# Kernel optimization log

Measured on AMD Instinct MI355X. Metric: run time of the kernel, lower is better.

## Reference

```python
import jax, jax.numpy as jnp
import numpy as np

B, S, C, HEADS = 1, 4096, 640, 8
AH, AW = 64, 64            # attn-resolution grid, AH*AW == S
MH, MW = 512, 512          # full-res mask size
NEG = -1e9                 # finite large negative (safe for fully-masked rows)


def nearest_resize(x, h, w):
    # torch F.interpolate(mode='nearest'): idx = floor(i * H_in / H_out)
    H, W = x.shape[-2], x.shape[-1]
    ri = (jnp.arange(h) * H) // h
    ci = (jnp.arange(w) * W) // w
    return x[..., ri, :][..., :, ci]


def sdpa(q, k, v, mask, heads):
    # q,k,v: [B,S,C]; mask: [B,1,S,S] bool (True = attend), broadcasts over heads
    b, s, c = q.shape
    d = c // heads
    qh = q.reshape(b, s, heads, d).transpose(0, 2, 1, 3)  # bhsd
    kh = k.reshape(b, s, heads, d).transpose(0, 2, 1, 3)
    vh = v.reshape(b, s, heads, d).transpose(0, 2, 1, 3)
    scores = jnp.einsum('bhqd,bhkd->bhqk', qh, kh) / jnp.sqrt(jnp.asarray(d, qh.dtype))
    scores = jnp.where(mask, scores, NEG)
    attn = jax.nn.softmax(scores, axis=-1)
    out = jnp.einsum('bhqk,bhkd->bhqd', attn, vh)
    return out.transpose(0, 2, 1, 3).reshape(b, s, c)


def setup_inputs():
    key = jax.random.key(0)
    ks = jax.random.split(key, 14)
    std = 1.0 / np.sqrt(C)
    w = lambda k: (jax.random.normal(k, (C, C), jnp.float32) * std)
    return {
        'hidden_states': jax.random.normal(ks[0], (B, S, C), jnp.float32),
        'mask': jax.random.randint(ks[1], (B, 1, MH, MW), 0, 4, jnp.int32),
        'inpainting_mask': jax.random.randint(ks[2], (B, 1, MH, MW), 0, 2, jnp.int32),
        'Wq': w(ks[3]), 'Wk': w(ks[4]), 'Wv': w(ks[5]),
        'Wq_ent': w(ks[6]), 'Wk_ent': w(ks[7]), 'Wv_ent': w(ks[8]),
        'Wq_out': w(ks[9]), 'Wk_out': w(ks[10]), 'Wv_out': w(ks[11]),
        'Wo': w(ks[12]),
    }


def reference(hidden_states, mask, inpainting_mask, Wq, Wk, Wv,
              Wq_ent, Wk_ent, Wv_ent, Wq_out, Wk_out, Wv_out, Wo):
    residual = hidden_states
    b, s, c = hidden_states.shape

    # --- interpolation-derived masks (kept as [B,1,S,S]; broadcasts over heads) ---
    m = nearest_resize(mask, AH, AW).reshape(b, 1, s)                 # entity labels
    attn_mask = m[:, :, :, None] == m[:, :, None, :]                  # same-entity [B,1,S,S]
    im = nearest_resize(inpainting_mask, AH, AW).reshape(b, 1, s)
    outside_key = (im[:, :, None, :] == 0)                            # [B,1,1,S]
    attn_mask_outside = attn_mask & outside_key                       # [B,1,S,S]

    # --- projections ---
    q = hidden_states @ Wq.T
    k = hidden_states @ Wk.T
    v = hidden_states @ Wv.T
    q_e = hidden_states @ Wq_ent.T
    k_e = hidden_states @ Wk_ent.T
    v_e = hidden_states @ Wv_ent.T
    q_o = hidden_states @ Wq_out.T
    k_o = hidden_states @ Wk_out.T
    v_o = hidden_states @ Wv_out.T

    # --- three SDPA branches ---
    hs_orig = sdpa(q, k, v, attn_mask, HEADS)            # original attention
    hs_ent = sdpa(q_e, k_e, v_e, attn_mask, 1)           # entity attention (1 head)
    hs_out = sdpa(q_o, k_o, v_o, attn_mask_outside, HEADS)  # outside attention

    hs = hs_orig + hs_ent + hs_out
    return hs @ Wo.T + residual
```

## Files before the change

kernel.cpp:

```cpp
#include <hip/hip_runtime.h>
#include <cstdint>

typedef __attribute__((ext_vector_type(8))) short bf16x8;
typedef __attribute__((ext_vector_type(4))) short bf16x4;
typedef __attribute__((ext_vector_type(4))) float f32x4;

#define S_LEN 4096
#define CDIM  640
#define NPROJ 5760

__device__ __forceinline__ f32x4 mfma16(bf16x4 a, bf16x4 b, f32x4 c){
#if defined(__HIP_DEVICE_COMPILE__) && __HIP_DEVICE_COMPILE__
  return __builtin_amdgcn_mfma_f32_16x16x16bf16_1k(a, b, c, 0, 0, 0);
#else
  (void)a; (void)b;
  return c;
#endif
}

__device__ __forceinline__ void gload_lds(const unsigned short* g, unsigned short* l){
#if defined(__HIP_DEVICE_COMPILE__) && __HIP_DEVICE_COMPILE__
  __builtin_amdgcn_global_load_lds((const __attribute__((address_space(1))) unsigned int*)g,
                                   (__attribute__((address_space(3))) unsigned int*)l, 16, 0, 0);
#else
  (void)g; (void)l;
#endif
}

__device__ __forceinline__ unsigned short f2bf(float f){
  union { float f; uint32_t u; } v; v.f = f;
  uint32_t u = v.u;
  return (unsigned short)((u + 0x7fffu + ((u >> 16) & 1u)) >> 16);
}
__device__ __forceinline__ float b2f(unsigned short h){
  union { uint32_t u; float f; } v; v.u = ((uint32_t)h) << 16;
  return v.f;
}

__global__ void k_labels(const int* __restrict__ mask, const int* __restrict__ inp,
                         int* __restrict__ labels){
  int s = blockIdx.x * 256 + threadIdx.x;
  if (s >= S_LEN) return;
  int y = s >> 6, x = s & 63;
  int off = (y * 8) * 512 + x * 8;
  int m = mask[off] & 0xff;
  int o = (inp[off] == 0) ? 0x100 : 0;
  labels[s] = m | o;
}

__global__ void k_hist(const int* __restrict__ labels, int* __restrict__ boff, int* __restrict__ cnt){
  __shared__ int h[4];
  if (threadIdx.x < 4) h[threadIdx.x] = 0;
  __syncthreads();
  for (int s = threadIdx.x; s < S_LEN; s += 256) atomicAdd(&h[labels[s] & 3], 1);
  __syncthreads();
  if (threadIdx.x == 0){
    int a = 0;
    for (int c = 0; c < 4; c++){ boff[c] = a; a += h[c]; }
    boff[4] = a;
  }
  if (threadIdx.x < 4) cnt[threadIdx.x] = 0;
}

__global__ void k_perm(const int* __restrict__ labels, const int* __restrict__ boff,
                       int* __restrict__ cnt, int* __restrict__ perm,
                       int* __restrict__ inv, int* __restrict__ labP){
  int s = blockIdx.x * 256 + threadIdx.x;
  if (s >= S_LEN) return;
  int lab = labels[s];
  int c = lab & 3;
  int pos = boff[c] + atomicAdd(&cnt[c], 1);
  perm[pos] = s; inv[s] = pos; labP[pos] = lab;
}

__global__ void k_tiles(const int* __restrict__ labP, const int* __restrict__ boff,
                        int4* __restrict__ qtinfo, float* __restrict__ rowsum){
  int t = threadIdx.x;
  __shared__ int nkt[32];
  if (t < 32){
    int c0 = labP[t * 128] & 3, c1 = labP[t * 128 + 127] & 3;
    int lo = boff[c0] & ~127, hi = (boff[c1 + 1] + 127) & ~127;
    qtinfo[t].x = lo; qtinfo[t].y = hi; qtinfo[t].w = 0;
    nkt[t] = (hi - lo) >> 7;
  }
  __syncthreads();
  if (t == 0){
    int a = 0;
    for (int i = 0; i < 32; i++){ qtinfo[i].z = a; a += nkt[i]; }
  }
  for (int s = t; s < S_LEN; s += 256) rowsum[s] = 0.f;
}

__global__ void k_cvt_hs(const float* __restrict__ src, unsigned short* __restrict__ dst, int n){
  int idx = (blockIdx.x * 256 + threadIdx.x) * 4;
  if (idx >= n) return;
  float4 v = *(const float4*)(src + idx);
  ushort4 o;
  o.x = f2bf(v.x); o.y = f2bf(v.y); o.z = f2bf(v.z); o.w = f2bf(v.w);
  *(ushort4*)(dst + idx) = o;
}

struct WPtrs { const float* w[10]; };

__global__ void k_cvt_w(WPtrs p, unsigned short* __restrict__ dst){
  int e = (blockIdx.x * 256 + threadIdx.x) * 4;
  if (e >= 10 * 409600) return;
  int a = e / 409600, r = e % 409600;
  float sc = (a == 0 || a == 6) ? 0.11180339887498948f
           : (a == 3 ? 0.03952847075210474f : 1.0f);
  float4 v = *(const float4*)(p.w[a] + r);
  ushort4 o;
  o.x = f2bf(v.x * sc); o.y = f2bf(v.y * sc); o.z = f2bf(v.z * sc); o.w = f2bf(v.w * sc);
  *(ushort4*)(dst + e) = o;
}

template<int EPI>
__global__ __launch_bounds__(256) void k_gemm(const unsigned short* __restrict__ A,
                                              const unsigned short* __restrict__ B,
                                              int M, int N, int K, int ldc,
                                              const int* __restrict__ rowmap,
                                              unsigned short* __restrict__ Cb,
                                              float* __restrict__ Cf,
                                              const float* __restrict__ resid){
  __shared__ __align__(16) unsigned short As[128 * 64];
  __shared__ __align__(16) unsigned short Bs[128 * 64];
  int m0 = blockIdx.y * 128, n0 = blockIdx.x * 128;
  int tid = threadIdx.x;
  int wid = tid >> 6, lane = tid & 63;
  int quad = lane >> 4, l16 = lane & 15;
  int wm = (wid >> 1) * 64, wn = (wid & 1) * 64;
  f32x4 acc[4][4];
#pragma unroll
  for (int i = 0; i < 4; i++)
#pragma unroll
    for (int j = 0; j < 4; j++) acc[i][j] = f32x4{0.f, 0.f, 0.f, 0.f};

  for (int k0 = 0; k0 < K; k0 += 64){
    __syncthreads();
#pragma unroll
    for (int u = 0; u < 4; u++){
      int c = tid + u * 256;
      int row = c >> 3, off = (c & 7) * 8;
      gload_lds(&A[(size_t)(m0 + row) * K + k0 + off], &As[c * 8]);
      gload_lds(&B[(size_t)(n0 + row) * K + k0 + off], &Bs[c * 8]);
    }
    __syncthreads();
#pragma unroll
    for (int ks = 0; ks < 2; ks++){
      bf16x8 af[4], bfr[4];
#pragma unroll
      for (int t = 0; t < 4; t++){
        af[t]  = *(const bf16x8*)(&As[(wm + t * 16 + l16) * 64 + ks * 32 + quad * 8]);
        bfr[t] = *(const bf16x8*)(&Bs[(wn + t * 16 + l16) * 64 + ks * 32 + quad * 8]);
      }
#pragma unroll
      for (int mt = 0; mt < 4; mt++)
#pragma unroll
        for (int nt = 0; nt < 4; nt++)
          acc[mt][nt] = __builtin_amdgcn_mfma_f32_16x16x32_bf16(af[mt], bfr[nt], acc[mt][nt], 0, 0, 0);
    }
  }
#pragma unroll
  for (int mt = 0; mt < 4; mt++)
#pragma unroll
    for (int nt = 0; nt < 4; nt++)
#pragma unroll
      for (int r = 0; r < 4; r++){
        int row = m0 + wm + mt * 16 + quad * 4 + r;
        int col = n0 + wn + nt * 16 + l16;
        float v = acc[mt][nt][r];
        if (EPI == 0){
          Cb[(size_t)rowmap[row] * ldc + col] = f2bf(v);
        } else {
          int ro = rowmap[row];
          Cf[(size_t)ro * ldc + col] = v + resid[(size_t)ro * ldc + col];
        }
      }
}

__global__ void k_transpose_v(const unsigned short* __restrict__ proj, unsigned short* __restrict__ vT){
  __shared__ unsigned short T[64][65];
  int z = blockIdx.z;
  int s0 = blockIdx.x * 64, c0 = blockIdx.y * 64;
  int colbase = 1280 + z * 1920 + c0;
  unsigned short* dst = vT + (size_t)z * CDIM * S_LEN;
  int tid = threadIdx.x;
  for (int i = tid; i < 64 * 64; i += 256){
    int r = i >> 6, c = i & 63;
    T[r][c] = proj[(size_t)(s0 + r) * NPROJ + colbase + c];
  }
  __syncthreads();
  for (int i = tid; i < 64 * 64; i += 256){
    int c = i >> 6, r = i & 63;
    dst[(size_t)(c0 + c) * S_LEN + s0 + r] = T[r][c];
  }
}

#define KP 84
#define VP 76
__global__ __launch_bounds__(256, 2) void k_attn80(const unsigned short* __restrict__ proj,
                                                   const unsigned short* __restrict__ vT,
                                                   const int* __restrict__ labP,
                                                   const int4* __restrict__ qtinfo,
                                                   unsigned short* __restrict__ outP){
  __shared__ __align__(16) unsigned short Ks[2][64 * KP];
  __shared__ __align__(16) unsigned short Vt[2][80 * VP];
  __shared__ __align__(16) int labk[2][64];
  int tid = threadIdx.x, wid = tid >> 6, lane = tid & 63;
  int quad = lane >> 4, l16 = lane & 15;
  int q0 = blockIdx.x * 128;
  int h  = blockIdx.y;
  bool OUTSIDE = (blockIdx.z == 1);
  int qc = (OUTSIDE ? 3840 : 0) + h * 80;
  int kc = (OUTSIDE ? 4480 : 640) + h * 80;
  const unsigned short* vTb = vT + (size_t)(OUTSIDE ? 2 : 0) * CDIM * S_LEN;
  int4 qi = qtinfo[blockIdx.x];
  int t0 = qi.x >> 6, t1 = qi.y >> 6;

  int qrow0 = q0 + wid * 32 + l16;
  int qrow1 = qrow0 + 16;
  bf16x4 qf0[5], qf1[5];
#pragma unroll
  for (int dc = 0; dc < 5; dc++){
    qf0[dc] = *(const bf16x4*)&proj[(size_t)qrow0 * NPROJ + qc + dc * 16 + quad * 4];
    qf1[dc] = *(const bf16x4*)&proj[(size_t)qrow1 * NPROJ + qc + dc * 16 + quad * 4];
  }
  int lq0 = labP[qrow0] & 0xff, lq1 = labP[qrow1] & 0xff;

  float lp0 = 0.f, lp1 = 0.f;
  f32x4 Oc0[5], Oc1[5];
#pragma unroll
  for (int t = 0; t < 5; t++){ Oc0[t] = f32x4{0.f,0.f,0.f,0.f}; Oc1[t] = f32x4{0.f,0.f,0.f,0.f}; }

  const int cS0 = tid, cS1 = tid + 256, cS2 = tid + 512, cS3 = tid + 768, cS4 = tid + 1024;
  const int kga0 = (cS0 / 20) * NPROJ + kc + (cS0 % 20) * 4;
  const int kga1 = (cS1 / 20) * NPROJ + kc + (cS1 % 20) * 4;
  const int kga2 = (cS2 / 20) * NPROJ + kc + (cS2 % 20) * 4;
  const int kga3 = (cS3 / 20) * NPROJ + kc + (cS3 % 20) * 4;
  const int kga4 = (cS4 / 20) * NPROJ + kc + (cS4 % 20) * 4;
  const int kls0 = (cS0 / 20) * KP + (cS0 % 20) * 4;
  const int kls1 = (cS1 / 20) * KP + (cS1 % 20) * 4;
  const int kls2 = (cS2 / 20) * KP + (cS2 % 20) * 4;
  const int kls3 = (cS3 / 20) * KP + (cS3 % 20) * 4;
  const int kls4 = (cS4 / 20) * KP + (cS4 % 20) * 4;
  const int vga0 = (h * 80 + (cS0 >> 4)) * S_LEN + (cS0 & 15) * 4;
  const int vga1 = (h * 80 + (cS1 >> 4)) * S_LEN + (cS1 & 15) * 4;
  const int vga2 = (h * 80 + (cS2 >> 4)) * S_LEN + (cS2 & 15) * 4;
  const int vga3 = (h * 80 + (cS3 >> 4)) * S_LEN + (cS3 & 15) * 4;
  const int vga4 = (h * 80 + (cS4 >> 4)) * S_LEN + (cS4 & 15) * 4;
  const int vls0 = (cS0 >> 4) * VP + (cS0 & 15) * 4;
  const int vls1 = (cS1 >> 4) * VP + (cS1 & 15) * 4;
  const int vls2 = (cS2 >> 4) * VP + (cS2 & 15) * 4;
  const int vls3 = (cS3 >> 4) * VP + (cS3 & 15) * 4;
  const int vls4 = (cS4 >> 4) * VP + (cS4 & 15) * 4;

  uint2 kr0, kr1, kr2, kr3, kr4, vr0, vr1, vr2, vr3, vr4;
  int lreg = 0;

#define LOADT(kt_) do {                                              \
    int _k0 = (kt_) * 64;                                            \
    size_t _kb = (size_t)_k0 * NPROJ;                                \
    kr0 = *(const uint2*)&proj[_kb + kga0];                          \
    kr1 = *(const uint2*)&proj[_kb + kga1];                          \
    kr2 = *(const uint2*)&proj[_kb + kga2];                          \
    kr3 = *(const uint2*)&proj[_kb + kga3];                          \
    kr4 = *(const uint2*)&proj[_kb + kga4];                          \
    vr0 = *(const uint2*)&vTb[(size_t)(vga0 + _k0)];                 \
    vr1 = *(const uint2*)&vTb[(size_t)(vga1 + _k0)];                 \
    vr2 = *(const uint2*)&vTb[(size_t)(vga2 + _k0)];                 \
    vr3 = *(const uint2*)&vTb[(size_t)(vga3 + _k0)];                 \
    vr4 = *(const uint2*)&vTb[(size_t)(vga4 + _k0)];                 \
    if (tid < 64) lreg = labP[_k0 + tid];                            \
  } while (0)

#define WRITET(b) do {                                               \
    *(uint2*)&Ks[b][kls0] = kr0;                                     \
    *(uint2*)&Ks[b][kls1] = kr1;                                     \
    *(uint2*)&Ks[b][kls2] = kr2;                                     \
    *(uint2*)&Ks[b][kls3] = kr3;                                     \
    *(uint2*)&Ks[b][kls4] = kr4;                                     \
    *(uint2*)&Vt[b][vls0] = vr0;                                     \
    *(uint2*)&Vt[b][vls1] = vr1;                                     \
    *(uint2*)&Vt[b][vls2] = vr2;                                     \
    *(uint2*)&Vt[b][vls3] = vr3;                                     \
    *(uint2*)&Vt[b][vls4] = vr4;                                     \
    if (tid < 64) labk[b][tid] = lreg;                               \
  } while (0)

  LOADT(t0);
  WRITET(0);
  if (t0 + 1 < t1) LOADT(t0 + 1);
  __syncthreads();

  int cur = 0;
  for (int kt = t0; kt < t1; kt++){
    int nxt = cur ^ 1;
    if (kt + 1 < t1){
      WRITET(nxt);
      if (kt + 2 < t1) LOADT(kt + 2);
    }

#pragma unroll
    for (int kg = 0; kg < 4; kg++){
      f32x4 sa0 = f32x4{0.f,0.f,0.f,0.f}, sa1 = f32x4{0.f,0.f,0.f,0.f};
#pragma unroll
      for (int dc = 0; dc < 5; dc++){
        bf16x4 kf = *(const bf16x4*)&Ks[cur][(kg * 16 + l16) * KP + dc * 16 + quad * 4];
        sa0 = mfma16(kf, qf0[dc], sa0);
        sa1 = mfma16(kf, qf1[dc], sa1);
      }
      int4 lk4 = *(const int4*)&labk[cur][kg * 16 + quad * 4];
      bool m0 = !OUTSIDE || (lk4.x & 0x100), m1 = !OUTSIDE || (lk4.y & 0x100);
      bool m2 = !OUTSIDE || (lk4.z & 0x100), m3 = !OUTSIDE || (lk4.w & 0x100);
      int k0l = lk4.x & 0xff, k1l = lk4.y & 0xff, k2l = lk4.z & 0xff, k3l = lk4.w & 0xff;
      bf16x4 pf0, pf1;
      {
        float p0 = (k0l == lq0 && m0) ? __expf(sa0[0]) : 0.f;
        float p1 = (k1l == lq0 && m1) ? __expf(sa0[1]) : 0.f;
        float p2 = (k2l == lq0 && m2) ? __expf(sa0[2]) : 0.f;
        float p3 = (k3l == lq0 && m3) ? __expf(sa0[3]) : 0.f;
        lp0 += (p0 + p1) + (p2 + p3);
        pf0[0] = (short)f2bf(p0); pf0[1] = (short)f2bf(p1);
        pf0[2] = (short)f2bf(p2); pf0[3] = (short)f2bf(p3);
      }
      {
        float p0 = (k0l == lq1 && m0) ? __expf(sa1[0]) : 0.f;
        float p1 = (k1l == lq1 && m1) ? __expf(sa1[1]) : 0.f;
        float p2 = (k2l == lq1 && m2) ? __expf(sa1[2]) : 0.f;
        float p3 = (k3l == lq1 && m3) ? __expf(sa1[3]) : 0.f;
        lp1 += (p0 + p1) + (p2 + p3);
        pf1[0] = (short)f2bf(p0); pf1[1] = (short)f2bf(p1);
        pf1[2] = (short)f2bf(p2); pf1[3] = (short)f2bf(p3);
      }
#pragma unroll
      for (int dt = 0; dt < 5; dt++){
        bf16x4 vf = *(const bf16x4*)&Vt[cur][(dt * 16 + l16) * VP + kg * 16 + quad * 4];
        Oc0[dt] = mfma16(vf, pf0, Oc0[dt]);
        Oc1[dt] = mfma16(vf, pf1, Oc1[dt]);
      }
    }
    __syncthreads();
    cur = nxt;
  }
#undef LOADT
#undef WRITET
  lp0 += __shfl_xor(lp0, 16); lp0 += __shfl_xor(lp0, 32);
  lp1 += __shfl_xor(lp1, 16); lp1 += __shfl_xor(lp1, 32);
  float iL0 = 1.f / lp0, iL1 = 1.f / lp1;
  unsigned short* dst = outP + (size_t)blockIdx.z * S_LEN * CDIM;
#pragma unroll
  for (int dt = 0; dt < 5; dt++){
    ushort4 o;
    o.x = f2bf(Oc0[dt][0] * iL0); o.y = f2bf(Oc0[dt][1] * iL0);
    o.z = f2bf(Oc0[dt][2] * iL0); o.w = f2bf(Oc0[dt][3] * iL0);
    *(ushort4*)&dst[(size_t)qrow0 * CDIM + h * 80 + dt * 16 + quad * 4] = o;
    o.x = f2bf(Oc1[dt][0] * iL1); o.y = f2bf(Oc1[dt][1] * iL1);
    o.z = f2bf(Oc1[dt][2] * iL1); o.w = f2bf(Oc1[dt][3] * iL1);
    *(ushort4*)&dst[(size_t)qrow1 * CDIM + h * 80 + dt * 16 + quad * 4] = o;
  }
}

__global__ __launch_bounds__(256) void k_ent_qk(const unsigned short* __restrict__ proj,
                                                const int* __restrict__ labP,
                                                const int4* __restrict__ qtinfo,
                                                unsigned short* __restrict__ Sbuf,
                                                float* __restrict__ rowsum){
  int qt = blockIdx.y;
  int4 qi = qtinfo[qt];
  int nkt = (qi.y - qi.x) >> 7;
  if ((int)blockIdx.x >= nkt) return;
  int m0 = qt * 128, n0 = qi.x + blockIdx.x * 128;
  __shared__ __align__(16) unsigned short As[128 * 64];
  __shared__ __align__(16) unsigned short Bs[128 * 64];
  __shared__ int lQ[128], lK[128];
  int tid = threadIdx.x, wid = tid >> 6, lane = tid & 63;
  int quad = lane >> 4, l16 = lane & 15;
  int wm = (wid >> 1) * 64, wn = (wid & 1) * 64;
  if (tid < 128) lQ[tid] = labP[m0 + tid] & 0xff;
  else           lK[tid - 128] = labP[n0 + tid - 128] & 0xff;
  f32x4 acc[4][4];
#pragma unroll
  for (int i = 0; i < 4; i++)
#pragma unroll
    for (int j = 0; j < 4; j++) acc[i][j] = f32x4{0.f, 0.f, 0.f, 0.f};

  for (int k0 = 0; k0 < 640; k0 += 64){
    __syncthreads();
#pragma unroll
    for (int u = 0; u < 4; u++){
      int c = tid + u * 256;
      int row = c >> 3, off = (c & 7) * 8;
      gload_lds(&proj[(size_t)(m0 + row) * NPROJ + 1920 + k0 + off], &As[c * 8]);
      gload_lds(&proj[(size_t)(n0 + row) * NPROJ + 2560 + k0 + off], &Bs[c * 8]);
    }
    __syncthreads();
#pragma unroll
    for (int ks = 0; ks < 2; ks++){
      bf16x8 af[4], bfr[4];
#pragma unroll
      for (int t = 0; t < 4; t++){
        af[t]  = *(const bf16x8*)(&As[(wm + t * 16 + l16) * 64 + ks * 32 + quad * 8]);
        bfr[t] = *(const bf16x8*)(&Bs[(wn + t * 16 + l16) * 64 + ks * 32 + quad * 8]);
      }
#pragma unroll
      for (int mt = 0; mt < 4; mt++)
#pragma unroll
        for (int nt = 0; nt < 4; nt++)
          acc[mt][nt] = __builtin_amdgcn_mfma_f32_16x16x32_bf16(af[mt], bfr[nt], acc[mt][nt], 0, 0, 0);
    }
  }
  unsigned short* St = Sbuf + ((size_t)(qi.z + blockIdx.x)) * 16384;
#pragma unroll
  for (int mt = 0; mt < 4; mt++)
#pragma unroll
    for (int r = 0; r < 4; r++){
      int lrow = wm + mt * 16 + quad * 4 + r;
      int myq = lQ[lrow];
      float psum = 0.f;
#pragma unroll
      for (int nt = 0; nt < 4; nt++){
        int lcol = wn + nt * 16 + l16;
        float p = (myq == lK[lcol]) ? __expf(acc[mt][nt][r]) : 0.f;
        St[lrow * 128 + lcol] = f2bf(p);
        psum += p;
      }
#pragma unroll
      for (int m = 1; m < 16; m <<= 1) psum += __shfl_xor(psum, m);
      if (l16 == 0) atomicAdd(&rowsum[m0 + lrow], psum);
    }
}

__global__ __launch_bounds__(256) void k_ent_pv(const unsigned short* __restrict__ Sbuf,
                                                const unsigned short* __restrict__ veT,
                                                const int4* __restrict__ qtinfo,
                                                const float* __restrict__ rowsum,
                                                const unsigned short* __restrict__ planes,
                                                unsigned short* __restrict__ attnS){
  int qt = blockIdx.y, d0 = blockIdx.x * 128;
  int4 qi = qtinfo[qt];
  int m0 = qt * 128;
  int nk = qi.y - qi.x;
  __shared__ __align__(16) unsigned short As[128 * 32];
  __shared__ __align__(16) unsigned short Bs[128 * 32];
  int tid = threadIdx.x, wid = tid >> 6, lane = tid & 63;
  int quad = lane >> 4, l16 = lane & 15;
  int wm = (wid >> 1) * 64, wn = (wid & 1) * 64;
  f32x4 acc[4][4];
#pragma unroll
  for (int i = 0; i < 4; i++)
#pragma unroll
    for (int j = 0; j < 4; j++) acc[i][j] = f32x4{0.f, 0.f, 0.f, 0.f};

  for (int kk = 0; kk < nk; kk += 32){
    const unsigned short* St = Sbuf + ((size_t)(qi.z + (kk >> 7))) * 16384;
    int kloc = kk & 127;
    __syncthreads();
#pragma unroll
    for (int u = 0; u < 2; u++){
      int c = tid + u * 256;
      int row = c >> 2, off = (c & 3) * 8;
      gload_lds(&St[row * 128 + kloc + off], &As[c * 8]);
      gload_lds(&veT[(size_t)(d0 + row) * S_LEN + qi.x + kk + off], &Bs[c * 8]);
    }
    __syncthreads();
    bf16x8 af[4], bfr[4];
#pragma unroll
    for (int t = 0; t < 4; t++){
      af[t]  = *(const bf16x8*)(&As[(wm + t * 16 + l16) * 32 + quad * 8]);
      bfr[t] = *(const bf16x8*)(&Bs[(wn + t * 16 + l16) * 32 + quad * 8]);
    }
#pragma unroll
    for (int mt = 0; mt < 4; mt++)
#pragma unroll
      for (int nt = 0; nt < 4; nt++)
        acc[mt][nt] = __builtin_amdgcn_mfma_f32_16x16x32_bf16(af[mt], bfr[nt], acc[mt][nt], 0, 0, 0);
  }
#pragma unroll
  for (int mt = 0; mt < 4; mt++)
#pragma unroll
    for (int r = 0; r < 4; r++){
      int row = m0 + wm + mt * 16 + quad * 4 + r;
      float invL = 1.f / rowsum[row];
#pragma unroll
      for (int nt = 0; nt < 4; nt++){
        int col = d0 + wn + nt * 16 + l16;
        size_t idx = (size_t)row * CDIM + col;
        float v = acc[mt][nt][r] * invL + b2f(planes[idx]) + b2f(planes[(size_t)S_LEN * CDIM + idx]);
        attnS[idx] = f2bf(v);
      }
    }
}

extern "C" void kernel_launch(void* const* d_in, const int* in_sizes, int n_in,
                              void* d_out, int out_size, void* d_ws, size_t ws_size,
                              hipStream_t stream){
  const float* hs  = (const float*)d_in[0];
  const int* mask  = (const int*)d_in[1];
  const int* inp   = (const int*)d_in[2];
  char* ws = (char*)d_ws;
  int*            labels  = (int*)(ws + 0);
  int*            boff    = (int*)(ws + 16384);
  int*            cnt     = (int*)(ws + 16640);
  int*            perm    = (int*)(ws + 16896);
  int*            inv     = (int*)(ws + 33280);
  int*            labP    = (int*)(ws + 49664);
  int4*           qtinfo  = (int4*)(ws + 66560);
  float*          rowsum  = (float*)(ws + 67072);
  unsigned short* hsb     = (unsigned short*)(ws + 131072);
  unsigned short* Wall    = (unsigned short*)(ws + 5373952);
  unsigned short* proj    = (unsigned short*)(ws + 13565952);
  unsigned short* vT      = (unsigned short*)(ws + 60751872);
  unsigned short* planes  = (unsigned short*)(ws + 76480512);
  unsigned short* Sbuf    = (unsigned short*)(ws + 86966272);
  unsigned short* attnS   = (unsigned short*)(ws + 120520704);
  unsigned short* Wob     = Wall + 9 * 409600;

  k_labels<<<16, 256, 0, stream>>>(mask, inp, labels);
  k_hist<<<1, 256, 0, stream>>>(labels, boff, cnt);
  k_perm<<<16, 256, 0, stream>>>(labels, boff, cnt, perm, inv, labP);
  k_tiles<<<1, 256, 0, stream>>>(labP, boff, qtinfo, rowsum);
  k_cvt_hs<<<(S_LEN * CDIM / 4 + 255) / 256, 256, 0, stream>>>(hs, hsb, S_LEN * CDIM);
  WPtrs wp;
  for (int i = 0; i < 10; i++) wp.w[i] = (const float*)d_in[3 + i];
  k_cvt_w<<<(10 * 409600 / 4 + 255) / 256, 256, 0, stream>>>(wp, Wall);

  k_gemm<0><<<dim3(45, 32), 256, 0, stream>>>(hsb, Wall, S_LEN, NPROJ, CDIM, NPROJ,
                                              inv, proj, nullptr, nullptr);
  k_transpose_v<<<dim3(64, 10, 3), 256, 0, stream>>>(proj, vT);

  k_attn80<<<dim3(32, 8, 2), 256, 0, stream>>>(proj, vT, labP, qtinfo, planes);

  k_ent_qk<<<dim3(32, 32), 256, 0, stream>>>(proj, labP, qtinfo, Sbuf, rowsum);
  k_ent_pv<<<dim3(5, 32), 256, 0, stream>>>(Sbuf, vT + (size_t)1 * CDIM * S_LEN,
                                            qtinfo, rowsum, planes, attnS);

  k_gemm<1><<<dim3(5, 32), 256, 0, stream>>>(attnS, Wob, S_LEN, CDIM, CDIM, CDIM,
                                             perm, nullptr, (float*)d_out, hs);
}
```

Measured before the change: 400.4 us.

## Split attention key range across two blocks and combine partials in a separate kernel

```diff
diff --git a/kernel.cpp b/kernel.cpp
--- a/kernel.cpp
+++ b/kernel.cpp
@@ -202,20 +202,26 @@
                                                    const unsigned short* __restrict__ vT,
                                                    const int* __restrict__ labP,
                                                    const int4* __restrict__ qtinfo,
-                                                   unsigned short* __restrict__ outP){
+                                                   unsigned short* __restrict__ opart,
+                                                   float* __restrict__ lpP){
   __shared__ __align__(16) unsigned short Ks[2][64 * KP];
   __shared__ __align__(16) unsigned short Vt[2][80 * VP];
   __shared__ __align__(16) int labk[2][64];
   int tid = threadIdx.x, wid = tid >> 6, lane = tid & 63;
   int quad = lane >> 4, l16 = lane & 15;
-  int q0 = blockIdx.x * 128;
+  int qt = blockIdx.x >> 1, half = blockIdx.x & 1;
+  int q0 = qt * 128;
   int h  = blockIdx.y;
   bool OUTSIDE = (blockIdx.z == 1);
   int qc = (OUTSIDE ? 3840 : 0) + h * 80;
   int kc = (OUTSIDE ? 4480 : 640) + h * 80;
   const unsigned short* vTb = vT + (size_t)(OUTSIDE ? 2 : 0) * CDIM * S_LEN;
-  int4 qi = qtinfo[blockIdx.x];
+  int4 qi = qtinfo[qt];
   int t0 = qi.x >> 6, t1 = qi.y >> 6;
+  int nt = t1 - t0;
+  int mid = t0 + ((nt + 1) >> 1);
+  int ta = half ? mid : t0;
+  int tb = half ? t1 : mid;
 
   int qrow0 = q0 + wid * 32 + l16;
   int qrow1 = qrow0 + 16;
@@ -287,17 +293,17 @@
     if (tid < 64) labk[b][tid] = lreg;                               \
   } while (0)
 
-  LOADT(t0);
+  LOADT(ta);
   WRITET(0);
-  if (t0 + 1 < t1) LOADT(t0 + 1);
+  if (ta + 1 < tb) LOADT(ta + 1);
   __syncthreads();
 
   int cur = 0;
-  for (int kt = t0; kt < t1; kt++){
+  for (int kt = ta; kt < tb; kt++){
     int nxt = cur ^ 1;
-    if (kt + 1 < t1){
+    if (kt + 1 < tb){
       WRITET(nxt);
-      if (kt + 2 < t1) LOADT(kt + 2);
+      if (kt + 2 < tb) LOADT(kt + 2);
     }
 
 #pragma unroll
@@ -346,18 +352,44 @@
 #undef WRITET
   lp0 += __shfl_xor(lp0, 16); lp0 += __shfl_xor(lp0, 32);
   lp1 += __shfl_xor(lp1, 16); lp1 += __shfl_xor(lp1, 32);
-  float iL0 = 1.f / lp0, iL1 = 1.f / lp1;
-  unsigned short* dst = outP + (size_t)blockIdx.z * S_LEN * CDIM;
+  int hz = half * 2 + (int)blockIdx.z;
+  if (quad == 0){
+    lpP[(size_t)(hz * 8 + h) * S_LEN + qrow0] = lp0;
+    lpP[(size_t)(hz * 8 + h) * S_LEN + qrow1] = lp1;
+  }
+  unsigned short* dst = opart + (size_t)hz * S_LEN * CDIM;
 #pragma unroll
   for (int dt = 0; dt < 5; dt++){
     ushort4 o;
-    o.x = f2bf(Oc0[dt][0] * iL0); o.y = f2bf(Oc0[dt][1] * iL0);
-    o.z = f2bf(Oc0[dt][2] * iL0); o.w = f2bf(Oc0[dt][3] * iL0);
+    o.x = f2bf(Oc0[dt][0]); o.y = f2bf(Oc0[dt][1]);
+    o.z = f2bf(Oc0[dt][2]); o.w = f2bf(Oc0[dt][3]);
     *(ushort4*)&dst[(size_t)qrow0 * CDIM + h * 80 + dt * 16 + quad * 4] = o;
-    o.x = f2bf(Oc1[dt][0] * iL1); o.y = f2bf(Oc1[dt][1] * iL1);
-    o.z = f2bf(Oc1[dt][2] * iL1); o.w = f2bf(Oc1[dt][3] * iL1);
+    o.x = f2bf(Oc1[dt][0]); o.y = f2bf(Oc1[dt][1]);
+    o.z = f2bf(Oc1[dt][2]); o.w = f2bf(Oc1[dt][3]);
     *(ushort4*)&dst[(size_t)qrow1 * CDIM + h * 80 + dt * 16 + quad * 4] = o;
   }
+}
+
+__global__ __launch_bounds__(256) void k_comb(const unsigned short* __restrict__ opart,
+                                              const float* __restrict__ lpP,
+                                              unsigned short* __restrict__ planes){
+  int i = blockIdx.x * 256 + threadIdx.x;
+  int z = blockIdx.y;
+  int qrow = i / 160, c4 = (i % 160) * 4;
+  int h = c4 / 80;
+  size_t o0 = ((size_t)(z)     * S_LEN + qrow) * CDIM + c4;
+  size_t o1 = ((size_t)(2 + z) * S_LEN + qrow) * CDIM + c4;
+  float lp = lpP[(size_t)(z * 8 + h) * S_LEN + qrow]
+           + lpP[(size_t)((2 + z) * 8 + h) * S_LEN + qrow];
+  float iL = 1.f / lp;
+  ushort4 a = *(const ushort4*)&opart[o0];
+  ushort4 b = *(const ushort4*)&opart[o1];
+  ushort4 o;
+  o.x = f2bf((b2f(a.x) + b2f(b.x)) * iL);
+  o.y = f2bf((b2f(a.y) + b2f(b.y)) * iL);
+  o.z = f2bf((b2f(a.z) + b2f(b.z)) * iL);
+  o.w = f2bf((b2f(a.w) + b2f(b.w)) * iL);
+  *(ushort4*)&planes[(size_t)z * S_LEN * CDIM + (size_t)qrow * CDIM + c4] = o;
 }
 
 __global__ __launch_bounds__(256) void k_ent_qk(const unsigned short* __restrict__ proj,
@@ -514,6 +546,8 @@
   unsigned short* Sbuf    = (unsigned short*)(ws + 86966272);
   unsigned short* attnS   = (unsigned short*)(ws + 120520704);
   unsigned short* Wob     = Wall + 9 * 409600;
+  unsigned short* opart   = Sbuf;
+  float*          lpP     = (float*)(ws + 86966272 + 20971520);
 
   k_labels<<<16, 256, 0, stream>>>(mask, inp, labels);
   k_hist<<<1, 256, 0, stream>>>(labels, boff, cnt);
@@ -528,7 +562,8 @@
                                               inv, proj, nullptr, nullptr);
   k_transpose_v<<<dim3(64, 10, 3), 256, 0, stream>>>(proj, vT);
 
-  k_attn80<<<dim3(32, 8, 2), 256, 0, stream>>>(proj, vT, labP, qtinfo, planes);
+  k_attn80<<<dim3(64, 8, 2), 256, 0, stream>>>(proj, vT, labP, qtinfo, opart, lpP);
+  k_comb<<<dim3(2560, 2), 256, 0, stream>>>(opart, lpP, planes);
 
   k_ent_qk<<<dim3(32, 32), 256, 0, stream>>>(proj, labP, qtinfo, Sbuf, rowsum);
   k_ent_pv<<<dim3(5, 32), 256, 0, stream>>>(Sbuf, vT + (size_t)1 * CDIM * S_LEN,
```

After: 411.7 us. 1.03x slower.
